# Optimization experiments

Hardware: AMD Instinct MI355X
Metric: run time of the kernel (lower is better)

The kernel has to match this reference:

```python
import jax, jax.numpy as jnp
from jax import lax
import numpy as np

KS = 7       # kernel_size
STRIDE = 2
PAD = KS // 2  # -inf padding (morphological identity) => out = ceil(H/stride)


def _parabolic_kernel(t):
    # z_i = linspace(-ks//2 + 1, ks//2, ks) -> centered offsets, e.g. [-3..3] for ks=7
    z_i = jnp.linspace(-(KS // 2), KS // 2, KS, dtype=jnp.float32)
    z_c = z_i[:, None] ** 2 + z_i[None, :] ** 2      # (KS, KS)
    # identical across channels (repeat_interleave of the same 2D kernel)
    return -z_c / (4.0 * t)


def setup_inputs() -> dict:
    key = jax.random.key(0)
    k1, k2 = jax.random.split(key)
    f = jax.random.normal(k1, (16, 128, 256, 256), dtype=jnp.float32)
    t = jnp.asarray(0.5, dtype=jnp.float32)
    return {"f": f, "t": t}


def reference(f, t):
    # Max-plus (morphological dilation) pooling with learned parabolic structuring element:
    # out[b,c,i,j] = max_{u,v} f[b,c, i*s + u - PAD, j*s + v - PAD] + h[u,v]
    B, C, H, W = f.shape
    h = _parabolic_kernel(t)                         # (KS, KS)
    Ho = (H + 2 * PAD - KS) // STRIDE + 1
    Wo = (W + 2 * PAD - KS) // STRIDE + 1
    neg_inf = jnp.asarray(-jnp.inf, f.dtype)
    fp = jnp.pad(f, ((0, 0), (0, 0), (PAD, PAD), (PAD, PAD)), constant_values=neg_inf)
    out = jnp.full((B, C, Ho, Wo), neg_inf, dtype=f.dtype)
    for u in range(KS):          # small fixed KS*KS loop; each iter is a strided slice + fused max
        for v in range(KS):
            win = lax.slice(
                fp,
                (0, 0, u, v),
                (B, C, u + STRIDE * (Ho - 1) + 1, v + STRIDE * (Wo - 1) + 1),
                (1, 1, STRIDE, STRIDE),
            )  # (B, C, Ho, Wo)
            out = jnp.maximum(out, win + h[u, v])
    return out
```

## Files before the change

### kernel.cpp

```cpp
#include <hip/hip_runtime.h>


#define H 256
#define W 256
#define HO 128
#define WO 128
#define TH 16
#define VPAD 4
#define VSTRIDE 276

__device__ __forceinline__ float4 f4max(float4 a, float4 b) {
    return make_float4(fmaxf(a.x, b.x), fmaxf(a.y, b.y), fmaxf(a.z, b.z), fmaxf(a.w, b.w));
}
__device__ __forceinline__ float4 f4adds(float4 a, float s) {
    return make_float4(a.x + s, a.y + s, a.z + s, a.w + s);
}

__global__ __launch_bounds__(512, 6)
void pp_kernel(const float* __restrict__ f, const float* __restrict__ tptr,
               float* __restrict__ out) {
    __shared__ __align__(16) float v_[TH * VSTRIDE];

    const int tid = threadIdx.x;
    const int bid = blockIdx.x;
    const int lid   = (bid & 7) * 2048 + (bid >> 3);
    const int plane = lid >> 3;
    const int strip = lid & 7;
    const int i0    = strip * TH;

    const float tv  = tptr[0];
    const float inv = 1.0f / (4.0f * tv);
    const float h0 = -9.0f * inv, h1 = -4.0f * inv, h2 = -1.0f * inv;
    const float NEG = -__builtin_inff();

    const float* __restrict__ fplane = f + (size_t)plane * (H * W);

    if (tid < 32) {
        const int r   = tid & 15;
        const int off = (tid < 16) ? 0 : (VPAD + W);
        *(float4*)(&v_[r * VSTRIDE + off]) = make_float4(NEG, NEG, NEG, NEG);
    }

    {
        const int x4    = (tid & 63) * 4;
        const int ipair = tid >> 6;
        const int ib    = 2 * ipair;
        const int gy0   = 2 * (i0 + ib) - 3;

        float4 r[9];
#pragma unroll
        for (int k = 0; k < 9; ++k) {
            const int cy = min(max(gy0 + k, 0), H - 1);
            r[k] = *(const float4*)(fplane + cy * W + x4);
        }

        float4 vA, vB;
        if (gy0 >= 0 && gy0 + 8 <= H - 1) {
            vA = f4max(f4max(f4adds(f4max(r[0], r[6]), h0),
                             f4adds(f4max(r[1], r[5]), h1)),
                       f4max(f4adds(f4max(r[2], r[4]), h2), r[3]));
            vB = f4max(f4max(f4adds(f4max(r[2], r[8]), h0),
                             f4adds(f4max(r[3], r[7]), h1)),
                       f4max(f4adds(f4max(r[4], r[6]), h2), r[5]));
        } else {
            const float hu[7] = {h0, h1, h2, 0.0f, h2, h1, h0};
            float4 a = make_float4(NEG, NEG, NEG, NEG);
            float4 b = make_float4(NEG, NEG, NEG, NEG);
#pragma unroll
            for (int u = 0; u < 7; ++u) {
                const int gyA = gy0 + u;
                const int gyB = gy0 + 2 + u;
                const float hA = (gyA >= 0 && gyA < H) ? hu[u] : NEG;
                const float hB = (gyB >= 0 && gyB < H) ? hu[u] : NEG;
                a = f4max(a, f4adds(r[u], hA));
                b = f4max(b, f4adds(r[u + 2], hB));
            }
            vA = a; vB = b;
        }

        *(float4*)(&v_[(ib)     * VSTRIDE + VPAD + x4]) = vA;
        *(float4*)(&v_[(ib + 1) * VSTRIDE + VPAD + x4]) = vB;
    }
    __syncthreads();

    {
        const int i  = tid >> 5;
        const int jg = tid & 31;
        const int c0 = 4 * jg;
        const float* p = &v_[i * VSTRIDE + 2 * c0];
        const float4 a = *(const float4*)(p);
        const float4 b = *(const float4*)(p + 4);
        const float4 c = *(const float4*)(p + 8);
        const float4 d = *(const float4*)(p + 12);
        const float s[16] = {a.x, a.y, a.z, a.w, b.x, b.y, b.z, b.w,
                             c.x, c.y, c.z, c.w, d.x, d.y, d.z, d.w};
        float4 o;
        float* op = (float*)&o;
#pragma unroll
        for (int dd = 0; dd < 4; ++dd) {
            const float m0 = fmaxf(s[2 * dd + 1], s[2 * dd + 7]) + h0;
            const float m1 = fmaxf(s[2 * dd + 2], s[2 * dd + 6]) + h1;
            const float m2 = fmaxf(s[2 * dd + 3], s[2 * dd + 5]) + h2;
            op[dd] = fmaxf(fmaxf(m0, m1), fmaxf(m2, s[2 * dd + 4]));
        }
        float* __restrict__ orow = out + (size_t)plane * (HO * WO) + (size_t)(i0 + i) * WO;
        *(float4*)(orow + c0) = o;
    }
}

extern "C" void kernel_launch(void* const* d_in, const int* in_sizes, int n_in,
                              void* d_out, int out_size, void* d_ws, size_t ws_size,
                              hipStream_t stream) {
    const float* f = (const float*)d_in[0];
    const float* t = (const float*)d_in[1];
    float* out = (float*)d_out;
    pp_kernel<<<dim3(2048 * 8), dim3(512), 0, stream>>>(f, t, out);
}
```

Measured before the change: 710.7 us.

## Process two row strips per block and prefetch the second strip's loads

```diff
diff --git a/kernel.cpp b/kernel.cpp
--- a/kernel.cpp
+++ b/kernel.cpp
@@ -16,6 +16,58 @@
     return make_float4(a.x + s, a.y + s, a.z + s, a.w + s);
 }
 
+__device__ __forceinline__ void vcompute(const float4 r[9], int gy0,
+                                         float h0, float h1, float h2, float NEG,
+                                         float4& vA, float4& vB) {
+    if (gy0 >= 0 && gy0 + 8 <= H - 1) {
+        vA = f4max(f4max(f4adds(f4max(r[0], r[6]), h0),
+                         f4adds(f4max(r[1], r[5]), h1)),
+                   f4max(f4adds(f4max(r[2], r[4]), h2), r[3]));
+        vB = f4max(f4max(f4adds(f4max(r[2], r[8]), h0),
+                         f4adds(f4max(r[3], r[7]), h1)),
+                   f4max(f4adds(f4max(r[4], r[6]), h2), r[5]));
+    } else {
+        const float hu[7] = {h0, h1, h2, 0.0f, h2, h1, h0};
+        float4 a = make_float4(NEG, NEG, NEG, NEG);
+        float4 b = make_float4(NEG, NEG, NEG, NEG);
+#pragma unroll
+        for (int u = 0; u < 7; ++u) {
+            const int gyA = gy0 + u;
+            const int gyB = gy0 + 2 + u;
+            const float hA = (gyA >= 0 && gyA < H) ? hu[u] : NEG;
+            const float hB = (gyB >= 0 && gyB < H) ? hu[u] : NEG;
+            a = f4max(a, f4adds(r[u], hA));
+            b = f4max(b, f4adds(r[u + 2], hB));
+        }
+        vA = a; vB = b;
+    }
+}
+
+__device__ __forceinline__ void hpass_store(const float* __restrict__ v_, int tid,
+                                            float h0, float h1, float h2,
+                                            float* __restrict__ oplane, int i0) {
+    const int i  = tid >> 5;
+    const int jg = tid & 31;
+    const int c0 = 4 * jg;
+    const float* p = &v_[i * VSTRIDE + 2 * c0];
+    const float4 a = *(const float4*)(p);
+    const float4 b = *(const float4*)(p + 4);
+    const float4 c = *(const float4*)(p + 8);
+    const float4 d = *(const float4*)(p + 12);
+    const float s[16] = {a.x, a.y, a.z, a.w, b.x, b.y, b.z, b.w,
+                         c.x, c.y, c.z, c.w, d.x, d.y, d.z, d.w};
+    float4 o;
+    float* op = (float*)&o;
+#pragma unroll
+    for (int dd = 0; dd < 4; ++dd) {
+        const float m0 = fmaxf(s[2 * dd + 1], s[2 * dd + 7]) + h0;
+        const float m1 = fmaxf(s[2 * dd + 2], s[2 * dd + 6]) + h1;
+        const float m2 = fmaxf(s[2 * dd + 3], s[2 * dd + 5]) + h2;
+        op[dd] = fmaxf(fmaxf(m0, m1), fmaxf(m2, s[2 * dd + 4]));
+    }
+    *(float4*)(oplane + (size_t)(i0 + i) * WO + c0) = o;
+}
+
 __global__ __launch_bounds__(512, 6)
 void pp_kernel(const float* __restrict__ f, const float* __restrict__ tptr,
                float* __restrict__ out) {
@@ -23,10 +75,11 @@
 
     const int tid = threadIdx.x;
     const int bid = blockIdx.x;
-    const int lid   = (bid & 7) * 2048 + (bid >> 3);
-    const int plane = lid >> 3;
-    const int strip = lid & 7;
-    const int i0    = strip * TH;
+    const int lid   = (bid & 7) * 1024 + (bid >> 3);
+    const int plane = lid >> 2;
+    const int ss    = lid & 3;
+    const int i0a   = ss * 32;
+    const int i0b   = i0a + TH;
 
     const float tv  = tptr[0];
     const float inv = 1.0f / (4.0f * tv);
@@ -34,6 +87,7 @@
     const float NEG = -__builtin_inff();
 
     const float* __restrict__ fplane = f + (size_t)plane * (H * W);
+    float* __restrict__ oplane = out + (size_t)plane * (HO * WO);
 
     if (tid < 32) {
         const int r   = tid & 15;
@@ -41,71 +95,45 @@
         *(float4*)(&v_[r * VSTRIDE + off]) = make_float4(NEG, NEG, NEG, NEG);
     }
 
+    const int x4    = (tid & 63) * 4;
+    const int ib    = (tid >> 6) * 2;
+    const int lofs0 = ib * VSTRIDE + VPAD + x4;
+
+    const int gy0a = 2 * (i0a + ib) - 3;
+    float4 r0[9];
+#pragma unroll
+    for (int k = 0; k < 9; ++k) {
+        const int cy = min(max(gy0a + k, 0), H - 1);
+        r0[k] = *(const float4*)(fplane + cy * W + x4);
+    }
     {
-        const int x4    = (tid & 63) * 4;
-        const int ipair = tid >> 6;
-        const int ib    = 2 * ipair;
-        const int gy0   = 2 * (i0 + ib) - 3;
-
-        float4 r[9];
-#pragma unroll
-        for (int k = 0; k < 9; ++k) {
-            const int cy = min(max(gy0 + k, 0), H - 1);
-            r[k] = *(const float4*)(fplane + cy * W + x4);
-        }
-
         float4 vA, vB;
-        if (gy0 >= 0 && gy0 + 8 <= H - 1) {
-            vA = f4max(f4max(f4adds(f4max(r[0], r[6]), h0),
-                             f4adds(f4max(r[1], r[5]), h1)),
-                       f4max(f4adds(f4max(r[2], r[4]), h2), r[3]));
-            vB = f4max(f4max(f4adds(f4max(r[2], r[8]), h0),
-                             f4adds(f4max(r[3], r[7]), h1)),
-                       f4max(f4adds(f4max(r[4], r[6]), h2), r[5]));
-        } else {
-            const float hu[7] = {h0, h1, h2, 0.0f, h2, h1, h0};
-            float4 a = make_float4(NEG, NEG, NEG, NEG);
-            float4 b = make_float4(NEG, NEG, NEG, NEG);
-#pragma unroll
-            for (int u = 0; u < 7; ++u) {
-                const int gyA = gy0 + u;
-                const int gyB = gy0 + 2 + u;
-                const float hA = (gyA >= 0 && gyA < H) ? hu[u] : NEG;
-                const float hB = (gyB >= 0 && gyB < H) ? hu[u] : NEG;
-                a = f4max(a, f4adds(r[u], hA));
-                b = f4max(b, f4adds(r[u + 2], hB));
-            }
-            vA = a; vB = b;
-        }
-
-        *(float4*)(&v_[(ib)     * VSTRIDE + VPAD + x4]) = vA;
-        *(float4*)(&v_[(ib + 1) * VSTRIDE + VPAD + x4]) = vB;
+        vcompute(r0, gy0a, h0, h1, h2, NEG, vA, vB);
+        *(float4*)(&v_[lofs0])           = vA;
+        *(float4*)(&v_[lofs0 + VSTRIDE]) = vB;
     }
     __syncthreads();
 
+    const int gy0b = 2 * (i0b + ib) - 3;
+    float4 r1[9];
+#pragma unroll
+    for (int k = 0; k < 9; ++k) {
+        const int cy = min(max(gy0b + k, 0), H - 1);
+        r1[k] = *(const float4*)(fplane + cy * W + x4);
+    }
+
+    hpass_store(v_, tid, h0, h1, h2, oplane, i0a);
+    __syncthreads();
+
     {
-        const int i  = tid >> 5;
-        const int jg = tid & 31;
-        const int c0 = 4 * jg;
-        const float* p = &v_[i * VSTRIDE + 2 * c0];
-        const float4 a = *(const float4*)(p);
-        const float4 b = *(const float4*)(p + 4);
-        const float4 c = *(const float4*)(p + 8);
-        const float4 d = *(const float4*)(p + 12);
-        const float s[16] = {a.x, a.y, a.z, a.w, b.x, b.y, b.z, b.w,
-                             c.x, c.y, c.z, c.w, d.x, d.y, d.z, d.w};
-        float4 o;
-        float* op = (float*)&o;
-#pragma unroll
-        for (int dd = 0; dd < 4; ++dd) {
-            const float m0 = fmaxf(s[2 * dd + 1], s[2 * dd + 7]) + h0;
-            const float m1 = fmaxf(s[2 * dd + 2], s[2 * dd + 6]) + h1;
-            const float m2 = fmaxf(s[2 * dd + 3], s[2 * dd + 5]) + h2;
-            op[dd] = fmaxf(fmaxf(m0, m1), fmaxf(m2, s[2 * dd + 4]));
-        }
-        float* __restrict__ orow = out + (size_t)plane * (HO * WO) + (size_t)(i0 + i) * WO;
-        *(float4*)(orow + c0) = o;
+        float4 vA, vB;
+        vcompute(r1, gy0b, h0, h1, h2, NEG, vA, vB);
+        *(float4*)(&v_[lofs0])           = vA;
+        *(float4*)(&v_[lofs0 + VSTRIDE]) = vB;
     }
+    __syncthreads();
+
+    hpass_store(v_, tid, h0, h1, h2, oplane, i0b);
 }
 
 extern "C" void kernel_launch(void* const* d_in, const int* in_sizes, int n_in,
@@ -114,5 +142,5 @@
     const float* f = (const float*)d_in[0];
     const float* t = (const float*)d_in[1];
     float* out = (float*)d_out;
-    pp_kernel<<<dim3(2048 * 8), dim3(512), 0, stream>>>(f, t, out);
+    pp_kernel<<<dim3(2048 * 4), dim3(512), 0, stream>>>(f, t, out);
 }
```

New measurement: 718.3 us. No clear change (+1.1%).

## Eliminate shared-memory staging by computing horizontal pass from per-thread register halos

Applied to the files above, without the earlier changes.

```diff
diff --git a/kernel.cpp b/kernel.cpp
--- a/kernel.cpp
+++ b/kernel.cpp
@@ -5,9 +5,6 @@
 #define W 256
 #define HO 128
 #define WO 128
-#define TH 16
-#define VPAD 4
-#define VSTRIDE 276
 
 __device__ __forceinline__ float4 f4max(float4 a, float4 b) {
     return make_float4(fmaxf(a.x, b.x), fmaxf(a.y, b.y), fmaxf(a.z, b.z), fmaxf(a.w, b.w));
@@ -16,17 +13,15 @@
     return make_float4(a.x + s, a.y + s, a.z + s, a.w + s);
 }
 
-__global__ __launch_bounds__(512, 6)
+__global__ __launch_bounds__(256, 3)
 void pp_kernel(const float* __restrict__ f, const float* __restrict__ tptr,
                float* __restrict__ out) {
-    __shared__ __align__(16) float v_[TH * VSTRIDE];
-
     const int tid = threadIdx.x;
     const int bid = blockIdx.x;
     const int lid   = (bid & 7) * 2048 + (bid >> 3);
     const int plane = lid >> 3;
     const int strip = lid & 7;
-    const int i0    = strip * TH;
+    const int i0    = strip * 16;
 
     const float tv  = tptr[0];
     const float inv = 1.0f / (4.0f * tv);
@@ -34,36 +29,36 @@
     const float NEG = -__builtin_inff();
 
     const float* __restrict__ fplane = f + (size_t)plane * (H * W);
+    float* __restrict__ oplane = out + (size_t)plane * (HO * WO);
 
-    if (tid < 32) {
-        const int r   = tid & 15;
-        const int off = (tid < 16) ? 0 : (VPAD + W);
-        *(float4*)(&v_[r * VSTRIDE + off]) = make_float4(NEG, NEG, NEG, NEG);
-    }
+    const int p   = tid >> 5;
+    const int jg  = tid & 31;
+    const int gy0 = 2 * (i0 + 2 * p) - 3;
+    const int gxb = 8 * jg - 4;
 
-    {
-        const int x4    = (tid & 63) * 4;
-        const int ipair = tid >> 6;
-        const int ib    = 2 * ipair;
-        const int gy0   = 2 * (i0 + ib) - 3;
+    const bool interior = (gy0 >= 0) && (gy0 + 8 <= H - 1);
+    float hu[7];
+    hu[0] = h0; hu[1] = h1; hu[2] = h2; hu[3] = 0.0f; hu[4] = h2; hu[5] = h1; hu[6] = h0;
 
+    float4 vA[4], vB[4];
+#pragma unroll
+    for (int g = 0; g < 4; ++g) {
+        const int cx = min(max(gxb + 4 * g, 0), W - 4);
+        const float* colp = fplane + cx;
         float4 r[9];
 #pragma unroll
         for (int k = 0; k < 9; ++k) {
             const int cy = min(max(gy0 + k, 0), H - 1);
-            r[k] = *(const float4*)(fplane + cy * W + x4);
+            r[k] = *(const float4*)(colp + cy * W);
         }
-
-        float4 vA, vB;
-        if (gy0 >= 0 && gy0 + 8 <= H - 1) {
-            vA = f4max(f4max(f4adds(f4max(r[0], r[6]), h0),
-                             f4adds(f4max(r[1], r[5]), h1)),
-                       f4max(f4adds(f4max(r[2], r[4]), h2), r[3]));
-            vB = f4max(f4max(f4adds(f4max(r[2], r[8]), h0),
-                             f4adds(f4max(r[3], r[7]), h1)),
-                       f4max(f4adds(f4max(r[4], r[6]), h2), r[5]));
+        if (interior) {
+            vA[g] = f4max(f4max(f4adds(f4max(r[0], r[6]), h0),
+                                f4adds(f4max(r[1], r[5]), h1)),
+                          f4max(f4adds(f4max(r[2], r[4]), h2), r[3]));
+            vB[g] = f4max(f4max(f4adds(f4max(r[2], r[8]), h0),
+                                f4adds(f4max(r[3], r[7]), h1)),
+                          f4max(f4adds(f4max(r[4], r[6]), h2), r[5]));
         } else {
-            const float hu[7] = {h0, h1, h2, 0.0f, h2, h1, h0};
             float4 a = make_float4(NEG, NEG, NEG, NEG);
             float4 b = make_float4(NEG, NEG, NEG, NEG);
 #pragma unroll
@@ -75,36 +70,35 @@
                 a = f4max(a, f4adds(r[u], hA));
                 b = f4max(b, f4adds(r[u + 2], hB));
             }
-            vA = a; vB = b;
+            vA[g] = a; vB[g] = b;
         }
+    }
 
-        *(float4*)(&v_[(ib)     * VSTRIDE + VPAD + x4]) = vA;
-        *(float4*)(&v_[(ib + 1) * VSTRIDE + VPAD + x4]) = vB;
-    }
-    __syncthreads();
+    if (jg == 0)  { vA[0] = make_float4(NEG, NEG, NEG, NEG); vB[0] = vA[0]; }
+    if (jg == 31) { vA[3] = make_float4(NEG, NEG, NEG, NEG); vB[3] = vA[3]; }
 
     {
-        const int i  = tid >> 5;
-        const int jg = tid & 31;
-        const int c0 = 4 * jg;
-        const float* p = &v_[i * VSTRIDE + 2 * c0];
-        const float4 a = *(const float4*)(p);
-        const float4 b = *(const float4*)(p + 4);
-        const float4 c = *(const float4*)(p + 8);
-        const float4 d = *(const float4*)(p + 12);
-        const float s[16] = {a.x, a.y, a.z, a.w, b.x, b.y, b.z, b.w,
-                             c.x, c.y, c.z, c.w, d.x, d.y, d.z, d.w};
-        float4 o;
-        float* op = (float*)&o;
+        const float sA[16] = {vA[0].x, vA[0].y, vA[0].z, vA[0].w, vA[1].x, vA[1].y, vA[1].z, vA[1].w,
+                              vA[2].x, vA[2].y, vA[2].z, vA[2].w, vA[3].x, vA[3].y, vA[3].z, vA[3].w};
+        const float sB[16] = {vB[0].x, vB[0].y, vB[0].z, vB[0].w, vB[1].x, vB[1].y, vB[1].z, vB[1].w,
+                              vB[2].x, vB[2].y, vB[2].z, vB[2].w, vB[3].x, vB[3].y, vB[3].z, vB[3].w};
+        float4 oA, oB;
+        float* opA = (float*)&oA;
+        float* opB = (float*)&oB;
 #pragma unroll
         for (int dd = 0; dd < 4; ++dd) {
-            const float m0 = fmaxf(s[2 * dd + 1], s[2 * dd + 7]) + h0;
-            const float m1 = fmaxf(s[2 * dd + 2], s[2 * dd + 6]) + h1;
-            const float m2 = fmaxf(s[2 * dd + 3], s[2 * dd + 5]) + h2;
-            op[dd] = fmaxf(fmaxf(m0, m1), fmaxf(m2, s[2 * dd + 4]));
+            const float a0 = fmaxf(sA[2 * dd + 1], sA[2 * dd + 7]) + h0;
+            const float a1 = fmaxf(sA[2 * dd + 2], sA[2 * dd + 6]) + h1;
+            const float a2 = fmaxf(sA[2 * dd + 3], sA[2 * dd + 5]) + h2;
+            opA[dd] = fmaxf(fmaxf(a0, a1), fmaxf(a2, sA[2 * dd + 4]));
+            const float b0 = fmaxf(sB[2 * dd + 1], sB[2 * dd + 7]) + h0;
+            const float b1 = fmaxf(sB[2 * dd + 2], sB[2 * dd + 6]) + h1;
+            const float b2 = fmaxf(sB[2 * dd + 3], sB[2 * dd + 5]) + h2;
+            opB[dd] = fmaxf(fmaxf(b0, b1), fmaxf(b2, sB[2 * dd + 4]));
         }
-        float* __restrict__ orow = out + (size_t)plane * (HO * WO) + (size_t)(i0 + i) * WO;
-        *(float4*)(orow + c0) = o;
+        const int orow = i0 + 2 * p;
+        *(float4*)(oplane + (size_t)orow * WO + 4 * jg)       = oA;
+        *(float4*)(oplane + (size_t)(orow + 1) * WO + 4 * jg) = oB;
     }
 }
 
@@ -114,5 +108,5 @@
     const float* f = (const float*)d_in[0];
     const float* t = (const float*)d_in[1];
     float* out = (float*)d_out;
-    pp_kernel<<<dim3(2048 * 8), dim3(512), 0, stream>>>(f, t, out);
+    pp_kernel<<<dim3(2048 * 8), dim3(256), 0, stream>>>(f, t, out);
 }
```

After: 768.1 us. 8.1% more time.
